# Optimization experiments

Measured on AMD Instinct MI355X. Metric: run time of the kernel, lower is better.

The kernel has to match this reference:

```python
import jax, jax.numpy as jnp
import numpy as np

N = 100000
E = 1600000
IN_DIM, HID, OUT = 256, 128, 64
K_HOPS = 5
ALPHA = 0.1
MLPA = 0.001


def setup_inputs() -> dict:
    key = jax.random.key(0)
    ks = jax.random.split(key, 20)
    s = 0.05
    inp = {
        "x": jax.random.normal(ks[0], (N, IN_DIM), jnp.float32),
        "edge_index": jax.random.randint(ks[1], (2, E), 0, N, jnp.int64),
        "edge_weight": jax.random.uniform(ks[2], (E,), jnp.float32),
        "A": jax.random.normal(ks[3], (N, 1), jnp.float32),
        # net1 MLP
        "m1_W1": jax.random.normal(ks[4], (IN_DIM, HID), jnp.float32) * s,
        "m1_b1": jnp.zeros((HID,), jnp.float32),
        "m1_W2": jax.random.normal(ks[5], (HID, OUT), jnp.float32) * s,
        "m1_b2": jnp.zeros((OUT,), jnp.float32),
        # net2 MLP
        "m2_W1": jax.random.normal(ks[6], (IN_DIM, HID), jnp.float32) * s,
        "m2_b1": jnp.zeros((HID,), jnp.float32),
        "m2_W2": jax.random.normal(ks[7], (HID, OUT), jnp.float32) * s,
        "m2_b2": jnp.zeros((OUT,), jnp.float32),
        # offset MLP (hidden*2)
        "off_W1": jax.random.normal(ks[8], (IN_DIM, 2 * HID), jnp.float32) * s,
        "off_b1": jnp.zeros((2 * HID,), jnp.float32),
        "off_W2": jax.random.normal(ks[9], (2 * HID, OUT), jnp.float32) * s,
        "off_b2": jnp.zeros((OUT,), jnp.float32),
        # mlp_A (A_dim=1 -> hidden*2 -> out)
        "A_W1": jax.random.normal(ks[10], (1, 2 * HID), jnp.float32) * s,
        "A_b1": jnp.zeros((2 * HID,), jnp.float32),
        "A_W2": jax.random.normal(ks[11], (2 * HID, OUT), jnp.float32) * s,
        "A_b2": jnp.zeros((OUT,), jnp.float32),
    }
    return inp


def _mlp2(x, W1, b1, W2, b2):
    return jax.nn.relu(x @ W1 + b1) @ W2 + b2


def _appnp(x, row, col, ew):
    # gcn_norm with added self loops (fill value 1)
    loop = jnp.arange(N, dtype=row.dtype)
    r = jnp.concatenate([row, loop])
    c = jnp.concatenate([col, loop])
    w = jnp.concatenate([ew, jnp.ones((N,), ew.dtype)])
    deg = jax.ops.segment_sum(w, c, num_segments=N)
    dinv = jnp.where(deg > 0, jax.lax.rsqrt(deg), 0.0)
    norm = dinv[r] * w * dinv[c]  # [E+N]
    h = x
    def step(xc, _):
        # gather source features, weight, scatter-add to targets
        agg = jax.ops.segment_sum(norm[:, None] * xc[r], c, num_segments=N)
        return agg * (1.0 - ALPHA) + ALPHA * h, None
    x, _ = jax.lax.scan(step, x, None, length=K_HOPS)
    return x


def reference(x, edge_index, edge_weight, A,
              m1_W1, m1_b1, m1_W2, m1_b2,
              m2_W1, m2_b1, m2_W2, m2_b2,
              off_W1, off_b1, off_W2, off_b2,
              A_W1, A_b1, A_W2, A_b2):
    row, col = edge_index[0], edge_index[1]
    # DualGNN edge-weight transforms, composed with APPNP_'s 1e-4 + 0.9999*w
    ew1 = 1e-4 + 0.9999 * (1e-5 + edge_weight * 0.99998)
    ew2 = 1e-4 + 0.9999 * (0.99999 - edge_weight * 0.99998)
    x1 = _appnp(_mlp2(x, m1_W1, m1_b1, m1_W2, m1_b2), row, col, ew1)
    x2 = _appnp(_mlp2(x, m2_W1, m2_b1, m2_W2, m2_b2), row, col, ew2)
    x_off = _mlp2(x, off_W1, off_b1, off_W2, off_b2)
    out = x1 - x2 + 0.001 * x_off
    out = out + MLPA * _mlp2(A, A_W1, A_b1, A_W2, A_b2)
    return jax.nn.log_softmax(out, axis=1)
```

## Files before the change

kernel.cpp:

```cpp
#include <hip/hip_runtime.h>
#include <stdint.h>

typedef unsigned int u32;
typedef unsigned short u16;
typedef unsigned long long u64;

#define IN_DIM 256

using bfrag = __attribute__((ext_vector_type(8))) short;
using f4 = __attribute__((ext_vector_type(4))) float;

__device__ __forceinline__ float bf2f(u16 u) {
  return __uint_as_float(((u32)u) << 16);
}
__device__ __forceinline__ u16 f2bf(float x) {
  u32 b = __float_as_uint(x);
  return (u16)((b + 0x7fffu + ((b >> 16) & 1u)) >> 16);
}
__device__ __forceinline__ f4 unpk(u32 a, u32 b) {
  return (f4){__uint_as_float(a << 16), __uint_as_float(a & 0xffff0000u),
              __uint_as_float(b << 16), __uint_as_float(b & 0xffff0000u)};
}

__global__ void k_pre(const int* __restrict__ ei, int E, int* flag,
                      u64* packed, int* cursor, int n, int NB,
                      const float* m1W1, const float* m2W1, const float* offW1,
                      const float* m1b1, const float* m2b1, const float* offb1,
                      const float* m1W2, const float* m2W2, const float* offW2,
                      const float* AW1, const float* AW2,
                      u16* WP1, u16* WP2a, u16* WP2b, u16* WP2o,
                      float* b1cat, float* Ppos, float* Pneg) {
  int bb = blockIdx.x, t = threadIdx.x;
  if (bb == 0) {
    __shared__ int ok;
    if (t == 0) ok = 1;
    __syncthreads();
    int m = (E < 512) ? E : 512;
    for (int i = t; i < m; i += 256)
      if (ei[2 * i + 1] != 0) ok = 0;
    __syncthreads();
    if (t == 0) flag[0] = ok;
    return;
  }
  if (bb < 1 + NB) {
    int i = (bb - 1) * 256 + t;
    if (i < n) { packed[i] = 0ULL; cursor[i] = 0; }
    return;
  }
  int b = bb - 1 - NB;
  if (b < 64) {
    int p = b * 256 + t;
    int l = p & 63, nt = (p >> 6) & 3, ks = (p >> 8) & 7, wvv = p >> 11;
    int col = wvv * 64 + nt * 16 + (l & 15);
    int k0 = ks * 32 + (l >> 4) * 8;
    u16 frag[8];
#pragma unroll
    for (int j = 0; j < 8; ++j) {
      int k = k0 + j;
      float v;
      if (col < 128) v = m1W1[k * 128 + col];
      else if (col < 256) v = m2W1[k * 128 + (col - 128)];
      else v = offW1[k * 256 + (col - 256)];
      frag[j] = f2bf(v);
    }
    *reinterpret_cast<uint4*>(WP1 + (size_t)p * 8) = *reinterpret_cast<const uint4*>(frag);
  } else if (b < 68) {
    int p = (b - 64) * 256 + t;
    int l = p & 63, nt = (p >> 6) & 3, ks = p >> 8;
    int col = nt * 16 + (l & 15);
    int k0 = ks * 32 + (l >> 4) * 8;
    u16 frag[8];
#pragma unroll
    for (int j = 0; j < 8; ++j) frag[j] = f2bf(m1W2[(k0 + j) * 64 + col]);
    *reinterpret_cast<uint4*>(WP2a + (size_t)p * 8) = *reinterpret_cast<const uint4*>(frag);
  } else if (b < 72) {
    int p = (b - 68) * 256 + t;
    int l = p & 63, nt = (p >> 6) & 3, ks = p >> 8;
    int col = nt * 16 + (l & 15);
    int k0 = ks * 32 + (l >> 4) * 8;
    u16 frag[8];
#pragma unroll
    for (int j = 0; j < 8; ++j) frag[j] = f2bf(m2W2[(k0 + j) * 64 + col]);
    *reinterpret_cast<uint4*>(WP2b + (size_t)p * 8) = *reinterpret_cast<const uint4*>(frag);
  } else if (b < 80) {
    int p = (b - 72) * 256 + t;
    int l = p & 63, nt = (p >> 6) & 3, ks = p >> 8;
    int col = nt * 16 + (l & 15);
    int k0 = ks * 32 + (l >> 4) * 8;
    u16 frag[8];
#pragma unroll
    for (int j = 0; j < 8; ++j) frag[j] = f2bf(offW2[(k0 + j) * 64 + col]);
    *reinterpret_cast<uint4*>(WP2o + (size_t)p * 8) = *reinterpret_cast<const uint4*>(frag);
  } else if (b < 82) {
    int g = (b - 80) * 256 + t;
    float v;
    if (g < 128) v = m1b1[g];
    else if (g < 256) v = m2b1[g - 128];
    else v = offb1[g - 256];
    b1cat[g] = v;
  } else {
    if (t < 64) {
      float sp = 0.f, sn = 0.f;
      for (int k = 0; k < 256; ++k) {
        float w = AW1[k];
        float w2 = AW2[k * 64 + t];
        sp += fmaxf(w, 0.f) * w2;
        sn += fmaxf(-w, 0.f) * w2;
      }
      Ppos[t] = sp; Pneg[t] = sn;
    }
  }
}

__global__ void k_dinv(const u64* __restrict__ packed, float2* d2v, float2* snv,
                       int* cnt, int n) {
  int i = blockIdx.x * 256 + threadIdx.x;
  if (i < n) {
    u64 pk = packed[i];
    int c = (int)(pk >> 44);
    u64 lo44 = pk & 0xFFFFFFFFFFFULL;
    float s1 = (float)(u32)(lo44 >> 32) + (float)(u32)(lo44 & 0xFFFFFFFFu) * (1.0f / 4294967296.0f);
    float d1 = 1.0f + s1;
    float d2 = 1.0f + 1.0001f * (float)c - s1;
    float r1 = rsqrtf(d1), r2 = rsqrtf(d2);
    d2v[i] = make_float2(r1, r2);
    snv[i] = make_float2(r1 * r1, r2 * r2);
    cnt[i] = c;
  }
}

__global__ void k_scan1(const int* __restrict__ cnt, int* row_ptr, int* bsum, int n) {
  __shared__ int s[256];
  int t = threadIdx.x;
  int base = blockIdx.x * 1024 + t * 4;
  int v[4]; int tsum = 0;
#pragma unroll
  for (int i = 0; i < 4; ++i) { int idx = base + i; v[i] = (idx < n) ? cnt[idx] : 0; tsum += v[i]; }
  s[t] = tsum; __syncthreads();
  for (int d = 1; d < 256; d <<= 1) {
    int tmp = (t >= d) ? s[t - d] : 0;
    __syncthreads();
    s[t] += tmp;
    __syncthreads();
  }
  int run = s[t] - tsum;
#pragma unroll
  for (int i = 0; i < 4; ++i) { int idx = base + i; if (idx < n) row_ptr[idx] = run; run += v[i]; }
  if (t == 255) bsum[blockIdx.x] = s[255];
}

__global__ void k_scan2(const int* bsum, int* boff, int nb) {
  __shared__ int s[128];
  int t = threadIdx.x;
  int v = (t < nb) ? bsum[t] : 0;
  s[t] = v; __syncthreads();
  for (int d = 1; d < 128; d <<= 1) {
    int tmp = (t >= d) ? s[t - d] : 0;
    __syncthreads();
    s[t] += tmp;
    __syncthreads();
  }
  if (t < nb) boff[t] = s[t] - v;
}

__global__ void k_scan3(int* row_ptr, const int* boff, int n, int E) {
  int t = threadIdx.x, b = blockIdx.x;
  int off = boff[b];
  int base = b * 1024 + t * 4;
#pragma unroll
  for (int i = 0; i < 4; ++i) { int idx = base + i; if (idx < n) row_ptr[idx] += off; }
  if (b == 0 && t == 0) row_ptr[n] = E;
}

__global__ void k_scatter(const int* __restrict__ ei, const float* __restrict__ ew,
                          const int* __restrict__ flag,
                          const float2* __restrict__ d2v,
                          const int* __restrict__ row_ptr, int* cursor, uint2* csr, int E) {
  int e = blockIdx.x * 256 + threadIdx.x;
  if (e >= E) return;
  int f = flag[0];
  int r = f ? ei[2 * e] : ei[e];
  int c = f ? ei[2 * (E + e)] : ei[E + e];
  float w = ew[e];
  float w1 = 1e-4f + 0.9999f * (1e-5f + w * 0.99998f);
  float w2 = 1e-4f + 0.9999f * (0.99999f - w * 0.99998f);
  float2 dr = d2v[r], dc = d2v[c];
  float n1 = dr.x * w1 * dc.x;
  float n2 = dr.y * w2 * dc.y;
  int p = row_ptr[c] + atomicAdd(&cursor[c], 1);
  csr[p] = make_uint2((u32)r, (u32)f2bf(n1) | ((u32)f2bf(n2) << 16));
}

__global__ __launch_bounds__(512, 3) void k_front(
    const float* __restrict__ xg, const u16* __restrict__ WP1, const float* __restrict__ b1cat,
    const u16* __restrict__ WP2a, const u16* __restrict__ WP2b, const u16* __restrict__ WP2o,
    const float* __restrict__ m1b2, const float* __restrict__ m2b2, const float* __restrict__ offb2,
    const float* __restrict__ Ab2, const float* __restrict__ Ppos, const float* __restrict__ Pneg,
    const float* __restrict__ Ag, u16* __restrict__ H0, u16* __restrict__ Bb, int n,
    const int* __restrict__ ei, const float* __restrict__ ew, const int* __restrict__ flag,
    u64* packed, int E, int EPB) {
  __shared__ __align__(16) char smem[65536];
  int tid = threadIdx.x;
  int bid = blockIdx.x;
  int m0 = bid * 64;
#pragma unroll
  for (int it = 0; it < 8; ++it) {
    int idx = it * 512 + tid;
    int row = idx >> 6, ch = idx & 63;
    int grow = m0 + row;
    float4 val = make_float4(0.f, 0.f, 0.f, 0.f);
    if (grow < n) val = *reinterpret_cast<const float4*>(xg + (size_t)grow * 256 + ch * 4);
    u32 lo = (u32)f2bf(val.x) | ((u32)f2bf(val.y) << 16);
    u32 hi2 = (u32)f2bf(val.z) | ((u32)f2bf(val.w) << 16);
    *reinterpret_cast<uint2*>(smem + row * 512 + ((ch * 8) ^ ((row & 7) << 4))) =
        make_uint2(lo, hi2);
  }
  __syncthreads();
  int wv = tid >> 6, ln = tid & 63;
  int l15 = ln & 15, lk = ln >> 4;
  int wn0 = wv * 64;
  f4 acc[4][4];
#pragma unroll
  for (int a = 0; a < 4; ++a)
#pragma unroll
    for (int b = 0; b < 4; ++b) acc[a][b] = (f4){0.f, 0.f, 0.f, 0.f};
#pragma unroll
  for (int ks = 0; ks < 8; ++ks) {
    bfrag a[4];
    int kb = ks * 64 + lk * 16;
#pragma unroll
    for (int mt = 0; mt < 4; ++mt) {
      int row = mt * 16 + l15;
      a[mt] = *reinterpret_cast<const bfrag*>(smem + row * 512 + (kb ^ ((row & 7) << 4)));
    }
#pragma unroll
    for (int nt = 0; nt < 4; ++nt) {
      bfrag b = *reinterpret_cast<const bfrag*>(
          WP1 + ((size_t)(((wv * 8 + ks) * 4 + nt) * 64 + ln) << 3));
#pragma unroll
      for (int mt = 0; mt < 4; ++mt)
        acc[mt][nt] = __builtin_amdgcn_mfma_f32_16x16x32_bf16(a[mt], b, acc[mt][nt], 0, 0, 0);
    }
  }
  __syncthreads();
#pragma unroll
  for (int nt = 0; nt < 4; ++nt) {
    int col = wn0 + nt * 16 + l15;
    float bias = b1cat[col];
#pragma unroll
    for (int mt = 0; mt < 4; ++mt) {
#pragma unroll
      for (int r = 0; r < 4; ++r) {
        int row = mt * 16 + lk * 4 + r;
        float v = fmaxf(acc[mt][nt][r] + bias, 0.f);
        *reinterpret_cast<u16*>(smem + row * 1024 + ((col * 2) ^ ((row & 7) << 4))) = f2bf(v);
      }
    }
  }
  __syncthreads();
  if (wv < 4) {
    f4 h1[4], h2[4];
#pragma unroll
    for (int i = 0; i < 4; ++i) { h1[i] = (f4){0,0,0,0}; h2[i] = (f4){0,0,0,0}; }
    int rowz = wv * 16 + l15;
    int swz = (rowz & 7) << 4;
#pragma unroll
    for (int ks = 0; ks < 4; ++ks) {
      int k1 = ks * 32 + lk * 8;
      bfrag a1 = *reinterpret_cast<const bfrag*>(smem + rowz * 1024 + ((k1 * 2) ^ swz));
      bfrag a2 = *reinterpret_cast<const bfrag*>(smem + rowz * 1024 + (((k1 + 128) * 2) ^ swz));
#pragma unroll
      for (int nt = 0; nt < 4; ++nt) {
        bfrag b1 = *reinterpret_cast<const bfrag*>(
            WP2a + ((size_t)((ks * 4 + nt) * 64 + ln) << 3));
        h1[nt] = __builtin_amdgcn_mfma_f32_16x16x32_bf16(a1, b1, h1[nt], 0, 0, 0);
        bfrag b2 = *reinterpret_cast<const bfrag*>(
            WP2b + ((size_t)((ks * 4 + nt) * 64 + ln) << 3));
        h2[nt] = __builtin_amdgcn_mfma_f32_16x16x32_bf16(a2, b2, h2[nt], 0, 0, 0);
      }
    }
    __syncthreads();
#pragma unroll
    for (int nt = 0; nt < 4; ++nt) {
      int col = nt * 16 + l15;
      float ba = m1b2[col], bbv = m2b2[col];
#pragma unroll
      for (int r = 0; r < 4; ++r) {
        int row = wv * 16 + lk * 4 + r;
        int swr = (row & 7) << 4;
        *reinterpret_cast<u16*>(smem + row * 256 + ((col * 2) ^ swr)) = f2bf(h1[nt][r] + ba);
        *reinterpret_cast<u16*>(smem + row * 256 + (((col + 64) * 2) ^ swr)) = f2bf(h2[nt][r] + bbv);
      }
    }
  } else {
    int wo = wv - 4;
    f4 ho[4];
#pragma unroll
    for (int i = 0; i < 4; ++i) ho[i] = (f4){0,0,0,0};
    int rowz = wo * 16 + l15;
    int swz = (rowz & 7) << 4;
#pragma unroll
    for (int ks = 0; ks < 8; ++ks) {
      int k1 = ks * 32 + lk * 8;
      bfrag a = *reinterpret_cast<const bfrag*>(smem + rowz * 1024 + (((k1 + 256) * 2) ^ swz));
#pragma unroll
      for (int nt = 0; nt < 4; ++nt) {
        bfrag b = *reinterpret_cast<const bfrag*>(
            WP2o + ((size_t)((ks * 4 + nt) * 64 + ln) << 3));
        ho[nt] = __builtin_amdgcn_mfma_f32_16x16x32_bf16(a, b, ho[nt], 0, 0, 0);
      }
    }
    __syncthreads();
#pragma unroll
    for (int nt = 0; nt < 4; ++nt) {
      int col = nt * 16 + l15;
      float bo = offb2[col];
      float pp = Ppos[col], pn = Pneg[col], ab2 = Ab2[col];
#pragma unroll
      for (int r = 0; r < 4; ++r) {
        int row = wo * 16 + lk * 4 + r;
        int grow = m0 + row;
        float av = (grow < n) ? Ag[grow] : 0.f;
        float mv = ab2 + (av > 0.f ? av * pp : (-av) * pn);
        *reinterpret_cast<u16*>(smem + 16384 + row * 128 + ((col * 2) ^ ((row & 7) << 4))) =
            f2bf(0.001f * (ho[nt][r] + bo) + 0.001f * mv);
      }
    }
  }
  __syncthreads();
#pragma unroll
  for (int i = 0; i < 2; ++i) {
    int idx = tid + i * 512;
    int row = idx >> 4, ch = idx & 15;
    if (m0 + row < n) {
      uint4 v = *reinterpret_cast<const uint4*>(smem + row * 256 + ((ch * 16) ^ ((row & 7) << 4)));
      *reinterpret_cast<uint4*>(H0 + (size_t)(m0 + row) * 128 + ch * 8) = v;
    }
  }
  {
    int row = tid >> 3, ch = tid & 7;
    if (m0 + row < n) {
      uint4 v = *reinterpret_cast<const uint4*>(smem + 16384 + row * 128 + ((ch * 16) ^ ((row & 7) << 4)));
      *reinterpret_cast<uint4*>(Bb + (size_t)(m0 + row) * 64 + ch * 8) = v;
    }
  }
  int f = flag[0];
  int ebase = bid * EPB;
  int eend = ebase + EPB; if (eend > E) eend = E;
  for (int e = ebase + tid; e < eend; e += 512) {
    int c = f ? ei[2 * (E + e)] : ei[E + e];
    float w = ew[e];
    float w1 = 1e-4f + 0.9999f * (1e-5f + w * 0.99998f);
    u64 add = (1ULL << 44) | (u64)(w1 * 4294967296.0f);
    atomicAdd(&packed[c], add);
  }
}

__global__ __launch_bounds__(256) void k_prop(
    const u16* __restrict__ Xsrc, const u16* __restrict__ H0, u16* __restrict__ Xdst,
    const uint2* __restrict__ csr, const int* __restrict__ row_ptr,
    const float2* __restrict__ snv, const u16* __restrict__ Bb, float* __restrict__ out,
    int n, int finalize) {
  int node = blockIdx.x * 4 + (threadIdx.x >> 6);
  if (node >= n) return;
  int ln = threadIdx.x & 63;
  int g = ln >> 4, q = ln & 15;
  bool isx2 = q >= 8;
  int e0 = row_ptr[node], e1 = row_ptr[node + 1];
  f4 a0 = {0.f, 0.f, 0.f, 0.f}, a1 = {0.f, 0.f, 0.f, 0.f};
  f4 b0 = {0.f, 0.f, 0.f, 0.f}, b1 = {0.f, 0.f, 0.f, 0.f};
  f4 c0 = {0.f, 0.f, 0.f, 0.f}, c1 = {0.f, 0.f, 0.f, 0.f};
  f4 d0 = {0.f, 0.f, 0.f, 0.f}, d1 = {0.f, 0.f, 0.f, 0.f};
  for (int base = e0; base < e1; base += 64) {
    int cnt = e1 - base; if (cnt > 64) cnt = 64;
    int idx = base + ln; if (idx >= e1) idx = e1 - 1;
    uint2 my = csr[idx];
    for (int j = 0; j < cnt; j += 16) {
      int s0 = j + g, s1 = j + 4 + g, s2 = j + 8 + g, s3 = j + 12 + g;
      int m0i = s0 < cnt ? s0 : cnt - 1;
      int m1i = s1 < cnt ? s1 : cnt - 1;
      int m2i = s2 < cnt ? s2 : cnt - 1;
      int m3i = s3 < cnt ? s3 : cnt - 1;
      u32 sx0 = (u32)__shfl((int)my.x, m0i);
      u32 sw0 = (u32)__shfl((int)my.y, m0i);
      u32 sx1 = (u32)__shfl((int)my.x, m1i);
      u32 sw1 = (u32)__shfl((int)my.y, m1i);
      u32 sx2 = (u32)__shfl((int)my.x, m2i);
      u32 sw2 = (u32)__shfl((int)my.y, m2i);
      u32 sx3 = (u32)__shfl((int)my.x, m3i);
      u32 sw3 = (u32)__shfl((int)my.y, m3i);
      uint4 u0 = *reinterpret_cast<const uint4*>(Xsrc + (size_t)sx0 * 128 + q * 8);
      uint4 u1 = *reinterpret_cast<const uint4*>(Xsrc + (size_t)sx1 * 128 + q * 8);
      uint4 u2 = *reinterpret_cast<const uint4*>(Xsrc + (size_t)sx2 * 128 + q * 8);
      uint4 u3 = *reinterpret_cast<const uint4*>(Xsrc + (size_t)sx3 * 128 + q * 8);
      float nn0 = (s0 < cnt) ? bf2f(isx2 ? (u16)(sw0 >> 16) : (u16)(sw0 & 0xffffu)) : 0.f;
      float nn1 = (s1 < cnt) ? bf2f(isx2 ? (u16)(sw1 >> 16) : (u16)(sw1 & 0xffffu)) : 0.f;
      float nn2 = (s2 < cnt) ? bf2f(isx2 ? (u16)(sw2 >> 16) : (u16)(sw2 & 0xffffu)) : 0.f;
      float nn3 = (s3 < cnt) ? bf2f(isx2 ? (u16)(sw3 >> 16) : (u16)(sw3 & 0xffffu)) : 0.f;
      a0 += nn0 * unpk(u0.x, u0.y);  a1 += nn0 * unpk(u0.z, u0.w);
      b0 += nn1 * unpk(u1.x, u1.y);  b1 += nn1 * unpk(u1.z, u1.w);
      c0 += nn2 * unpk(u2.x, u2.y);  c1 += nn2 * unpk(u2.z, u2.w);
      d0 += nn3 * unpk(u3.x, u3.y);  d1 += nn3 * unpk(u3.z, u3.w);
    }
  }
  a0 += b0 + c0 + d0; a1 += b1 + c1 + d1;
#pragma unroll
  for (int i = 0; i < 4; ++i) {
    a0[i] += __shfl_xor(a0[i], 16, 64);
    a0[i] += __shfl_xor(a0[i], 32, 64);
    a1[i] += __shfl_xor(a1[i], 16, 64);
    a1[i] += __shfl_xor(a1[i], 32, 64);
  }
  float2 snp = snv[node];
  float sn = isx2 ? snp.y : snp.x;
  uint4 us = *reinterpret_cast<const uint4*>(Xsrc + (size_t)node * 128 + q * 8);
  a0 += sn * unpk(us.x, us.y);
  a1 += sn * unpk(us.z, us.w);
  uint4 uh = *reinterpret_cast<const uint4*>(H0 + (size_t)node * 128 + q * 8);
  f4 hv0 = unpk(uh.x, uh.y), hv1 = unpk(uh.z, uh.w);
  f4 r0, r1;
#pragma unroll
  for (int i = 0; i < 4; ++i) {
    r0[i] = 0.9f * a0[i] + 0.1f * hv0[i];
    r1[i] = 0.9f * a1[i] + 0.1f * hv1[i];
  }
  if (!finalize) {
    if (g == 0) {
      uint4 o;
      o.x = (u32)f2bf(r0[0]) | ((u32)f2bf(r0[1]) << 16);
      o.y = (u32)f2bf(r0[2]) | ((u32)f2bf(r0[3]) << 16);
      o.z = (u32)f2bf(r1[0]) | ((u32)f2bf(r1[1]) << 16);
      o.w = (u32)f2bf(r1[2]) | ((u32)f2bf(r1[3]) << 16);
      *reinterpret_cast<uint4*>(Xdst + (size_t)node * 128 + q * 8) = o;
    }
  } else {
    f4 o0, o1;
#pragma unroll
    for (int i = 0; i < 4; ++i) {
      o0[i] = __shfl_xor(r0[i], 8, 64);
      o1[i] = __shfl_xor(r1[i], 8, 64);
    }
    uint4 ub = make_uint4(0, 0, 0, 0);
    if (q < 8) ub = *reinterpret_cast<const uint4*>(Bb + (size_t)node * 64 + q * 8);
    f4 bv0 = unpk(ub.x, ub.y), bv1 = unpk(ub.z, ub.w);
    f4 v0, v1;
#pragma unroll
    for (int i = 0; i < 4; ++i) {
      v0[i] = r0[i] - o0[i] + bv0[i];
      v1[i] = r1[i] - o1[i] + bv1[i];
    }
    float m = fmaxf(fmaxf(fmaxf(v0[0], v0[1]), fmaxf(v0[2], v0[3])),
                    fmaxf(fmaxf(v1[0], v1[1]), fmaxf(v1[2], v1[3])));
#pragma unroll
    for (int off = 1; off < 8; off <<= 1) m = fmaxf(m, __shfl_xor(m, off, 64));
    float s = __expf(v0[0] - m) + __expf(v0[1] - m) + __expf(v0[2] - m) + __expf(v0[3] - m) +
              __expf(v1[0] - m) + __expf(v1[1] - m) + __expf(v1[2] - m) + __expf(v1[3] - m);
#pragma unroll
    for (int off = 1; off < 8; off <<= 1) s += __shfl_xor(s, off, 64);
    float ls = m + __logf(s);
    if (g == 0 && q < 8) {
      float4 w0 = make_float4(v0[0] - ls, v0[1] - ls, v0[2] - ls, v0[3] - ls);
      float4 w1 = make_float4(v1[0] - ls, v1[1] - ls, v1[2] - ls, v1[3] - ls);
      *reinterpret_cast<float4*>(out + (size_t)node * 64 + q * 8) = w0;
      *reinterpret_cast<float4*>(out + (size_t)node * 64 + q * 8 + 4) = w1;
    }
  }
}

extern "C" void kernel_launch(void* const* d_in, const int* in_sizes, int n_in,
                              void* d_out, int out_size, void* d_ws, size_t ws_size,
                              hipStream_t stream) {
  const float* xg    = (const float*)d_in[0];
  const int* ei      = (const int*)d_in[1];
  const float* ewgt  = (const float*)d_in[2];
  const float* Ag    = (const float*)d_in[3];
  const float* m1W1  = (const float*)d_in[4];
  const float* m1b1  = (const float*)d_in[5];
  const float* m1W2  = (const float*)d_in[6];
  const float* m1b2  = (const float*)d_in[7];
  const float* m2W1  = (const float*)d_in[8];
  const float* m2b1  = (const float*)d_in[9];
  const float* m2W2  = (const float*)d_in[10];
  const float* m2b2  = (const float*)d_in[11];
  const float* offW1 = (const float*)d_in[12];
  const float* offb1 = (const float*)d_in[13];
  const float* offW2 = (const float*)d_in[14];
  const float* offb2 = (const float*)d_in[15];
  const float* AW1   = (const float*)d_in[16];
  const float* AW2   = (const float*)d_in[18];
  const float* Ab2   = (const float*)d_in[19];
  int n = in_sizes[0] / IN_DIM;
  int E = in_sizes[1] / 2;

  char* p = (char*)d_ws;
  auto alloc = [&](size_t bytes) { char* r = p; p += (bytes + 255) & ~(size_t)255; return r; };
  u16* H0    = (u16*)alloc((size_t)n * 128 * 2);
  u16* Xa    = (u16*)alloc((size_t)n * 128 * 2);
  u16* Xb    = (u16*)alloc((size_t)n * 128 * 2);
  u16* Bb    = (u16*)alloc((size_t)n * 64 * 2 + 256);
  uint2* csr = (uint2*)alloc((size_t)E * 8);
  u16* WP1   = (u16*)alloc((size_t)16384 * 16);
  u16* WP2a  = (u16*)alloc((size_t)1024 * 16);
  u16* WP2b  = (u16*)alloc((size_t)1024 * 16);
  u16* WP2o  = (u16*)alloc((size_t)2048 * 16);
  float* b1cat = (float*)alloc(512 * 4);
  float* Ppos  = (float*)alloc(64 * 4);
  float* Pneg  = (float*)alloc(64 * 4);
  u64* packed  = (u64*)alloc((size_t)n * 8);
  float2* d2v  = (float2*)alloc((size_t)n * 8);
  float2* snv  = (float2*)alloc((size_t)n * 8);
  int* cnt     = (int*)alloc((size_t)n * 4);
  int* cursor  = (int*)alloc((size_t)n * 4);
  int* row_ptr = (int*)alloc(((size_t)n + 1) * 4);
  int* bsum    = (int*)alloc(512);
  int* boff    = (int*)alloc(512);
  int* flag    = (int*)alloc(256);

  int nb256 = (n + 255) / 256;
  int eb = (E + 255) / 256;
  int nb1024 = (n + 1023) / 1024;
  int pb = (n + 3) / 4;
  int MB = (n + 63) / 64;
  int EPB = (E + MB - 1) / MB;

  k_pre<<<1 + nb256 + 83, 256, 0, stream>>>(ei, E, flag, packed, cursor, n, nb256,
                                            m1W1, m2W1, offW1, m1b1, m2b1, offb1,
                                            m1W2, m2W2, offW2, AW1, AW2,
                                            WP1, WP2a, WP2b, WP2o, b1cat, Ppos, Pneg);
  k_front<<<MB, 512, 0, stream>>>(xg, WP1, b1cat, WP2a, WP2b, WP2o,
                                  m1b2, m2b2, offb2, Ab2, Ppos, Pneg,
                                  Ag, H0, Bb, n, ei, ewgt, flag, packed, E, EPB);
  k_dinv<<<nb256, 256, 0, stream>>>(packed, d2v, snv, cnt, n);
  k_scan1<<<nb1024, 256, 0, stream>>>(cnt, row_ptr, bsum, n);
  k_scan2<<<1, 128, 0, stream>>>(bsum, boff, nb1024);
  k_scan3<<<nb1024, 256, 0, stream>>>(row_ptr, boff, n, E);
  k_scatter<<<eb, 256, 0, stream>>>(ei, ewgt, flag, d2v, row_ptr, cursor, csr, E);
  float* outp = (float*)d_out;
  k_prop<<<pb, 256, 0, stream>>>(H0, H0, Xa, csr, row_ptr, snv, Bb, outp, n, 0);
  k_prop<<<pb, 256, 0, stream>>>(Xa, H0, Xb, csr, row_ptr, snv, Bb, outp, n, 0);
  k_prop<<<pb, 256, 0, stream>>>(Xb, H0, Xa, csr, row_ptr, snv, Bb, outp, n, 0);
  k_prop<<<pb, 256, 0, stream>>>(Xa, H0, Xb, csr, row_ptr, snv, Bb, outp, n, 0);
  k_prop<<<pb, 256, 0, stream>>>(Xb, H0, Xa, csr, row_ptr, snv, Bb, outp, n, 1);
}
```

Measured before the change: 580.4 us.

## Reuse degree-atomic return as CSR slot and fuse dinv into scan

The degree-count atomic in k_front now keeps its returned old count as each edge's slot within its target row. k_scatter then computes its CSR position as row_ptr + slot, with no second round of atomics on a cursor array. The dinv computation moves into k_scan1, which drops one kernel launch and the cnt round trip. The cost is an extra E-sized int array that is written and then read, and the CSR order within a row now follows the first atomic's order.

After: 536.2 us, median of 2. 7.6% less time.

```diff
diff --git a/kernel.cpp b/kernel.cpp
--- a/kernel.cpp
+++ b/kernel.cpp
@@ -23,7 +23,7 @@
 }
 
 __global__ void k_pre(const int* __restrict__ ei, int E, int* flag,
-                      u64* packed, int* cursor, int n, int NB,
+                      u64* packed, int n, int NB,
                       const float* m1W1, const float* m2W1, const float* offW1,
                       const float* m1b1, const float* m2b1, const float* offb1,
                       const float* m1W2, const float* m2W2, const float* offW2,
@@ -44,7 +44,7 @@
   }
   if (bb < 1 + NB) {
     int i = (bb - 1) * 256 + t;
-    if (i < n) { packed[i] = 0ULL; cursor[i] = 0; }
+    if (i < n) packed[i] = 0ULL;
     return;
   }
   int b = bb - 1 - NB;
@@ -112,30 +112,29 @@
   }
 }
 
-__global__ void k_dinv(const u64* __restrict__ packed, float2* d2v, float2* snv,
-                       int* cnt, int n) {
-  int i = blockIdx.x * 256 + threadIdx.x;
-  if (i < n) {
-    u64 pk = packed[i];
-    int c = (int)(pk >> 44);
-    u64 lo44 = pk & 0xFFFFFFFFFFFULL;
-    float s1 = (float)(u32)(lo44 >> 32) + (float)(u32)(lo44 & 0xFFFFFFFFu) * (1.0f / 4294967296.0f);
-    float d1 = 1.0f + s1;
-    float d2 = 1.0f + 1.0001f * (float)c - s1;
-    float r1 = rsqrtf(d1), r2 = rsqrtf(d2);
-    d2v[i] = make_float2(r1, r2);
-    snv[i] = make_float2(r1 * r1, r2 * r2);
-    cnt[i] = c;
-  }
-}
-
-__global__ void k_scan1(const int* __restrict__ cnt, int* row_ptr, int* bsum, int n) {
+__global__ void k_scan1(const u64* __restrict__ packed, float2* d2v, float2* snv,
+                        int* row_ptr, int* bsum, int n) {
   __shared__ int s[256];
   int t = threadIdx.x;
   int base = blockIdx.x * 1024 + t * 4;
   int v[4]; int tsum = 0;
 #pragma unroll
-  for (int i = 0; i < 4; ++i) { int idx = base + i; v[i] = (idx < n) ? cnt[idx] : 0; tsum += v[i]; }
+  for (int i = 0; i < 4; ++i) {
+    int idx = base + i;
+    int c = 0;
+    if (idx < n) {
+      u64 pk = packed[idx];
+      c = (int)(pk >> 44);
+      u64 lo44 = pk & 0xFFFFFFFFFFFULL;
+      float s1 = (float)(u32)(lo44 >> 32) + (float)(u32)(lo44 & 0xFFFFFFFFu) * (1.0f / 4294967296.0f);
+      float d1 = 1.0f + s1;
+      float d2 = 1.0f + 1.0001f * (float)c - s1;
+      float r1 = rsqrtf(d1), r2 = rsqrtf(d2);
+      d2v[idx] = make_float2(r1, r2);
+      snv[idx] = make_float2(r1 * r1, r2 * r2);
+    }
+    v[i] = c; tsum += c;
+  }
   s[t] = tsum; __syncthreads();
   for (int d = 1; d < 256; d <<= 1) {
     int tmp = (t >= d) ? s[t - d] : 0;
@@ -173,9 +172,9 @@
 }
 
 __global__ void k_scatter(const int* __restrict__ ei, const float* __restrict__ ew,
-                          const int* __restrict__ flag,
+                          const int* __restrict__ flag, const int* __restrict__ slot,
                           const float2* __restrict__ d2v,
-                          const int* __restrict__ row_ptr, int* cursor, uint2* csr, int E) {
+                          const int* __restrict__ row_ptr, uint2* csr, int E) {
   int e = blockIdx.x * 256 + threadIdx.x;
   if (e >= E) return;
   int f = flag[0];
@@ -187,7 +186,7 @@
   float2 dr = d2v[r], dc = d2v[c];
   float n1 = dr.x * w1 * dc.x;
   float n2 = dr.y * w2 * dc.y;
-  int p = row_ptr[c] + atomicAdd(&cursor[c], 1);
+  int p = row_ptr[c] + slot[e];
   csr[p] = make_uint2((u32)r, (u32)f2bf(n1) | ((u32)f2bf(n2) << 16));
 }
 
@@ -198,7 +197,7 @@
     const float* __restrict__ Ab2, const float* __restrict__ Ppos, const float* __restrict__ Pneg,
     const float* __restrict__ Ag, u16* __restrict__ H0, u16* __restrict__ Bb, int n,
     const int* __restrict__ ei, const float* __restrict__ ew, const int* __restrict__ flag,
-    u64* packed, int E, int EPB) {
+    u64* packed, int* slot, int E, int EPB) {
   __shared__ __align__(16) char smem[65536];
   int tid = threadIdx.x;
   int bid = blockIdx.x;
@@ -352,7 +351,8 @@
     float w = ew[e];
     float w1 = 1e-4f + 0.9999f * (1e-5f + w * 0.99998f);
     u64 add = (1ULL << 44) | (u64)(w1 * 4294967296.0f);
-    atomicAdd(&packed[c], add);
+    u64 old = atomicAdd(&packed[c], add);
+    slot[e] = (int)(old >> 44);
   }
 }
 
@@ -499,6 +499,7 @@
   u16* Xb    = (u16*)alloc((size_t)n * 128 * 2);
   u16* Bb    = (u16*)alloc((size_t)n * 64 * 2 + 256);
   uint2* csr = (uint2*)alloc((size_t)E * 8);
+  int* slot  = (int*)alloc((size_t)E * 4);
   u16* WP1   = (u16*)alloc((size_t)16384 * 16);
   u16* WP2a  = (u16*)alloc((size_t)1024 * 16);
   u16* WP2b  = (u16*)alloc((size_t)1024 * 16);
@@ -509,8 +510,6 @@
   u64* packed  = (u64*)alloc((size_t)n * 8);
   float2* d2v  = (float2*)alloc((size_t)n * 8);
   float2* snv  = (float2*)alloc((size_t)n * 8);
-  int* cnt     = (int*)alloc((size_t)n * 4);
-  int* cursor  = (int*)alloc((size_t)n * 4);
   int* row_ptr = (int*)alloc(((size_t)n + 1) * 4);
   int* bsum    = (int*)alloc(512);
   int* boff    = (int*)alloc(512);
@@ -523,18 +522,17 @@
   int MB = (n + 63) / 64;
   int EPB = (E + MB - 1) / MB;
 
-  k_pre<<<1 + nb256 + 83, 256, 0, stream>>>(ei, E, flag, packed, cursor, n, nb256,
+  k_pre<<<1 + nb256 + 83, 256, 0, stream>>>(ei, E, flag, packed, n, nb256,
                                             m1W1, m2W1, offW1, m1b1, m2b1, offb1,
                                             m1W2, m2W2, offW2, AW1, AW2,
                                             WP1, WP2a, WP2b, WP2o, b1cat, Ppos, Pneg);
   k_front<<<MB, 512, 0, stream>>>(xg, WP1, b1cat, WP2a, WP2b, WP2o,
                                   m1b2, m2b2, offb2, Ab2, Ppos, Pneg,
-                                  Ag, H0, Bb, n, ei, ewgt, flag, packed, E, EPB);
-  k_dinv<<<nb256, 256, 0, stream>>>(packed, d2v, snv, cnt, n);
-  k_scan1<<<nb1024, 256, 0, stream>>>(cnt, row_ptr, bsum, n);
+                                  Ag, H0, Bb, n, ei, ewgt, flag, packed, slot, E, EPB);
+  k_scan1<<<nb1024, 256, 0, stream>>>(packed, d2v, snv, row_ptr, bsum, n);
   k_scan2<<<1, 128, 0, stream>>>(bsum, boff, nb1024);
   k_scan3<<<nb1024, 256, 0, stream>>>(row_ptr, boff, n, E);
-  k_scatter<<<eb, 256, 0, stream>>>(ei, ewgt, flag, d2v, row_ptr, cursor, csr, E);
+  k_scatter<<<eb, 256, 0, stream>>>(ei, ewgt, flag, slot, d2v, row_ptr, csr, E);
   float* outp = (float*)d_out;
   k_prop<<<pb, 256, 0, stream>>>(H0, H0, Xa, csr, row_ptr, snv, Bb, outp, n, 0);
   k_prop<<<pb, 256, 0, stream>>>(Xa, H0, Xb, csr, row_ptr, snv, Bb, outp, n, 0);
```
